# Kernel tuning notes

Hardware: AMD Instinct MI355X
Metric: run time of the kernel (lower is better)

Reference implementation:

```python
import jax, jax.numpy as jnp
import numpy as np

SIZE = (160, 192, 160)  # matches init_kwargs `size`


def _make_grid(size):
    # torch: meshgrid(arange(s) for s, indexing='ij'), stack last dim, flip last dim
    vecs = [jnp.arange(s, dtype=jnp.float32) for s in size]
    g = jnp.stack(jnp.meshgrid(*vecs, indexing='ij'), axis=-1)
    g = g[..., ::-1]  # last-dim order becomes (x, y, z) = (W, H, D) indices
    return g[None]    # [1, D, H, W, 3]


def _grid_sample_3d(src, locs):
    """Trilinear grid_sample, align_corners=True, padding_mode='zeros'.
    src: [B, C, D, H, W]; locs: [B, D, H, W, 3] in [-1,1], last dim (x,y,z)."""
    B, C, D, H, W = src.shape
    dims_m1 = jnp.array([W - 1, H - 1, D - 1], jnp.float32)
    px = (locs + 1.0) * 0.5 * dims_m1  # unnormalize (align_corners=True)
    x, y, z = px[..., 0], px[..., 1], px[..., 2]
    x0 = jnp.floor(x); y0 = jnp.floor(y); z0 = jnp.floor(z)
    fx, fy, fz = x - x0, y - y0, z - z0
    x0i = x0.astype(jnp.int32); y0i = y0.astype(jnp.int32); z0i = z0.astype(jnp.int32)

    def gather(src_b, iz, iy, ix):  # src_b: [C,D,H,W]; idx: [D,H,W]
        return src_b[:, iz, iy, ix]  # [C,D,H,W]

    out = jnp.zeros(src.shape, src.dtype)
    for dz in (0, 1):
        for dy in (0, 1):
            for dx in (0, 1):
                ix, iy, iz = x0i + dx, y0i + dy, z0i + dz
                valid = (ix >= 0) & (ix < W) & (iy >= 0) & (iy < H) & (iz >= 0) & (iz < D)
                w = ((fx if dx else 1.0 - fx)
                     * (fy if dy else 1.0 - fy)
                     * (fz if dz else 1.0 - fz))
                w = jnp.where(valid, w, 0.0)  # zero padding for OOB
                icx = jnp.clip(ix, 0, W - 1)
                icy = jnp.clip(iy, 0, H - 1)
                icz = jnp.clip(iz, 0, D - 1)
                v = jax.vmap(gather)(src, icz, icy, icx)  # [B,C,D,H,W]
                out = out + w[:, None] * v
    return out


def setup_inputs() -> dict:
    key = jax.random.key(0)
    k1, k2 = jax.random.split(key)
    B, C = 2, 2
    D, H, W = SIZE
    src = jax.random.normal(k1, (B, C, D, H, W), dtype=jnp.float32)
    flow = jax.random.normal(k2, (B, 3, D, H, W), dtype=jnp.float32)
    return {"src": src, "flow": flow}


def reference(src, flow):
    # order='image': no flip of flow channels
    flow = jnp.moveaxis(flow, 1, -1)                      # [B,D,H,W,3]
    grid = _make_grid(SIZE)                                # [1,D,H,W,3]
    s = jnp.array(SIZE, jnp.float32)[::-1] - 1.0           # [W-1,H-1,D-1]
    new_locs = 2.0 * ((grid + flow) / s - 0.5)             # normalized [-1,1]
    return _grid_sample_3d(src, new_locs)
```

## Files before the change

kernel.cpp:

```cpp
#include <hip/hip_runtime.h>

#define DD 160
#define HH 192
#define WW 160
#define SP (DD * HH * WW)
#define NB 2
#define NC 2

#define TX 32
#define TY 8
#define TZ 4
#define RXW 40
#define RYH 15
#define RZD 11
#define REGC (RZD * RYH * RXW)
#define NCHUNK (2 * REGC / 4)
#define NITER 13

#define NTX 5
#define NTY 24
#define NTZ 40
#define NTILES (NTX * NTY * NTZ * NB)
#define PER_XCD (NTILES / 8)

typedef float v2f __attribute__((ext_vector_type(2)));
typedef float v4f __attribute__((ext_vector_type(4)));

__device__ __forceinline__ v4f ld4_nt(const float* p) {
    return __builtin_nontemporal_load(reinterpret_cast<const v4f*>(p));
}
__device__ __forceinline__ void st4_nt(float* p, v4f v) {
    __builtin_nontemporal_store(v, reinterpret_cast<v4f*>(p));
}
__device__ __forceinline__ v2f ld2g(const float* p) {
    return *reinterpret_cast<const v2f*>(p);
}

__device__ __forceinline__ void sample_global(
    const float* __restrict__ s0, const float* __restrict__ s1,
    int x, int y, int z, float dx, float dy, float dz,
    float& a0, float& a1)
{
    float sx = (float)x + dx, sy = (float)y + dy, sz = (float)z + dz;
    float xf = floorf(sx), yf = floorf(sy), zf = floorf(sz);
    float fx = sx - xf, fy = sy - yf, fz = sz - zf;
    int x0 = (int)xf, y0 = (int)yf, z0 = (int)zf;
    int x1 = x0 + 1, y1 = y0 + 1, z1 = z0 + 1;

    float wx0 = (x0 >= 0 && x0 < WW) ? (1.0f - fx) : 0.0f;
    float wx1 = (x1 >= 0 && x1 < WW) ? fx : 0.0f;
    float wy0 = (y0 >= 0 && y0 < HH) ? (1.0f - fy) : 0.0f;
    float wy1 = (y1 >= 0 && y1 < HH) ? fy : 0.0f;
    float wz0 = (z0 >= 0 && z0 < DD) ? (1.0f - fz) : 0.0f;
    float wz1 = (z1 >= 0 && z1 < DD) ? fz : 0.0f;

    int p  = min(max(x0, 0), WW - 2);
    int i0 = min(max(x0, 0), WW - 1) - p;
    int i1 = min(max(x1, 0), WW - 1) - p;
    int cy0 = min(max(y0, 0), HH - 1), cy1 = min(max(y1, 0), HH - 1);
    int cz0 = min(max(z0, 0), DD - 1), cz1 = min(max(z1, 0), DD - 1);

    int o00 = (cz0 * HH + cy0) * WW + p;
    int o01 = (cz0 * HH + cy1) * WW + p;
    int o10 = (cz1 * HH + cy0) * WW + p;
    int o11 = (cz1 * HH + cy1) * WW + p;

    float w00 = wz0 * wy0, w01 = wz0 * wy1, w10 = wz1 * wy0, w11 = wz1 * wy1;

    v2f c0_00 = ld2g(s0 + o00); v2f c1_00 = ld2g(s1 + o00);
    v2f c0_01 = ld2g(s0 + o01); v2f c1_01 = ld2g(s1 + o01);
    v2f c0_10 = ld2g(s0 + o10); v2f c1_10 = ld2g(s1 + o10);
    v2f c0_11 = ld2g(s0 + o11); v2f c1_11 = ld2g(s1 + o11);

    #define PICK(v, i) ((i) ? (v).y : (v).x)
    float r0, r1;
    r0  = w00 * (wx0 * PICK(c0_00, i0) + wx1 * PICK(c0_00, i1));
    r1  = w00 * (wx0 * PICK(c1_00, i0) + wx1 * PICK(c1_00, i1));
    r0 += w01 * (wx0 * PICK(c0_01, i0) + wx1 * PICK(c0_01, i1));
    r1 += w01 * (wx0 * PICK(c1_01, i0) + wx1 * PICK(c1_01, i1));
    r0 += w10 * (wx0 * PICK(c0_10, i0) + wx1 * PICK(c0_10, i1));
    r1 += w10 * (wx0 * PICK(c1_10, i0) + wx1 * PICK(c1_10, i1));
    r0 += w11 * (wx0 * PICK(c0_11, i0) + wx1 * PICK(c0_11, i1));
    r1 += w11 * (wx0 * PICK(c1_11, i0) + wx1 * PICK(c1_11, i1));
    #undef PICK
    a0 = r0; a1 = r1;
}

__global__ __launch_bounds__(256, 3) void st_warp_kernel(
    const float* __restrict__ src,
    const float* __restrict__ flow,
    float* __restrict__ out)
{
    __shared__ float sbuf[2 * REGC];

    int u   = blockIdx.x;
    int tl  = (u & 7) * PER_XCD + (u >> 3);
    int tx  = tl % NTX;  int t2 = tl / NTX;
    int ty  = t2 % NTY;  int t3 = t2 / NTY;
    int tz  = t3 % NTZ;  int b  = t3 / NTZ;
    int X0 = tx * TX, Y0 = ty * TY, Z0 = tz * TZ;
    int tid = threadIdx.x;

    const float* sb = src + b * NC * SP;
    const float* s1g = sb + SP;

    v4f vals[NITER];
    int  laddr[NITER];
    #pragma unroll
    for (int i = 0; i < NITER; ++i) {
        int c = tid + i * 256;
        if (i < NITER - 1 || c < NCHUNK) {
            int ch  = (c >= REGC / 4) ? 1 : 0;
            int rem = c - ch * (REGC / 4);
            int lz  = rem / (RYH * RXW / 4);
            int r2  = rem - lz * (RYH * RXW / 4);
            int ly  = r2 / (RXW / 4);
            int lxc = r2 - ly * (RXW / 4);
            int mz = min(max(Z0 - 3 + lz, 0), DD - 1);
            int my = min(max(Y0 - 3 + ly, 0), HH - 1);
            int mx = X0 - 4 + lxc * 4;
            const float* p = sb + ch * SP + (mz * HH + my) * WW;
            v4f v;
            if (mx >= 0 && mx <= WW - 4) {
                v = *reinterpret_cast<const v4f*>(p + mx);
            } else {
                v.x = p[min(max(mx,     0), WW - 1)];
                v.y = p[min(max(mx + 1, 0), WW - 1)];
                v.z = p[min(max(mx + 2, 0), WW - 1)];
                v.w = p[min(max(mx + 3, 0), WW - 1)];
            }
            vals[i]  = v;
            laddr[i] = ch * REGC + (lz * RYH + ly) * RXW + lxc * 4;
        } else {
            laddr[i] = -1;
        }
    }

    int rr = tid >> 3;
    int xi = (tid & 7) << 2;
    int y = Y0 + (rr & 7);
    int z = Z0 + (rr >> 3);
    int x = X0 + xi;
    int fo = b * 3 * SP + (z * HH + y) * WW + x;
    v4f dxv = ld4_nt(flow + fo);
    v4f dyv = ld4_nt(flow + fo + SP);
    v4f dzv = ld4_nt(flow + fo + 2 * SP);

    #pragma unroll
    for (int i = 0; i < NITER; ++i)
        if (laddr[i] >= 0)
            *reinterpret_cast<v4f*>(&sbuf[laddr[i]]) = vals[i];
    __syncthreads();

    const float* c0 = sbuf;
    const float* c1 = sbuf + REGC;
    int rx0 = X0 - 4, ry0 = Y0 - 3, rz0 = Z0 - 3;

    float a0[4], a1[4];
    #pragma unroll
    for (int j = 0; j < 4; ++j) {
        float dx = dxv[j], dy = dyv[j], dz = dzv[j];
        bool inH = (dx >= -4.0f) & (dx < 4.0f) &
                   (dy >= -3.0f) & (dy < 4.0f) &
                   (dz >= -3.0f) & (dz < 4.0f);
        if (inH) {
            float sx = (float)(x + j) + dx;
            float sy = (float)y + dy;
            float sz = (float)z + dz;
            float xf = floorf(sx), yf = floorf(sy), zf = floorf(sz);
            float fx = sx - xf, fy = sy - yf, fz = sz - zf;
            int x0 = (int)xf, y0 = (int)yf, z0 = (int)zf;
            int x1 = x0 + 1, y1 = y0 + 1, z1 = z0 + 1;

            float wx0 = (x0 >= 0 && x0 < WW) ? (1.0f - fx) : 0.0f;
            float wx1 = (x1 >= 0 && x1 < WW) ? fx : 0.0f;
            float wy0 = (y0 >= 0 && y0 < HH) ? (1.0f - fy) : 0.0f;
            float wy1 = (y1 >= 0 && y1 < HH) ? fy : 0.0f;
            float wz0 = (z0 >= 0 && z0 < DD) ? (1.0f - fz) : 0.0f;
            float wz1 = (z1 >= 0 && z1 < DD) ? fz : 0.0f;

            int cx0 = min(max(x0, 0), WW - 1), cx1 = min(max(x1, 0), WW - 1);
            int cy0 = min(max(y0, 0), HH - 1), cy1 = min(max(y1, 0), HH - 1);
            int cz0 = min(max(z0, 0), DD - 1), cz1 = min(max(z1, 0), DD - 1);

            int pb = cx0 - rx0;
            int i1 = cx1 - cx0;
            int ly0 = cy0 - ry0, ly1 = cy1 - ry0;
            int lz0 = cz0 - rz0, lz1 = cz1 - rz0;

            int o00 = (lz0 * RYH + ly0) * RXW + pb;
            int o01 = (lz0 * RYH + ly1) * RXW + pb;
            int o10 = (lz1 * RYH + ly0) * RXW + pb;
            int o11 = (lz1 * RYH + ly1) * RXW + pb;

            float w00 = wz0 * wy0, w01 = wz0 * wy1;
            float w10 = wz1 * wy0, w11 = wz1 * wy1;

            float p00a = c0[o00], p00b = c0[o00 + 1];
            float q00a = c1[o00], q00b = c1[o00 + 1];
            float p01a = c0[o01], p01b = c0[o01 + 1];
            float q01a = c1[o01], q01b = c1[o01 + 1];
            float p10a = c0[o10], p10b = c0[o10 + 1];
            float q10a = c1[o10], q10b = c1[o10 + 1];
            float p11a = c0[o11], p11b = c0[o11 + 1];
            float q11a = c1[o11], q11b = c1[o11 + 1];

            #define SEL(a_, b_) ((i1) ? (b_) : (a_))
            float r0, r1;
            r0  = w00 * (wx0 * p00a + wx1 * SEL(p00a, p00b));
            r1  = w00 * (wx0 * q00a + wx1 * SEL(q00a, q00b));
            r0 += w01 * (wx0 * p01a + wx1 * SEL(p01a, p01b));
            r1 += w01 * (wx0 * q01a + wx1 * SEL(q01a, q01b));
            r0 += w10 * (wx0 * p10a + wx1 * SEL(p10a, p10b));
            r1 += w10 * (wx0 * q10a + wx1 * SEL(q10a, q10b));
            r0 += w11 * (wx0 * p11a + wx1 * SEL(p11a, p11b));
            r1 += w11 * (wx0 * q11a + wx1 * SEL(q11a, q11b));
            #undef SEL
            a0[j] = r0; a1[j] = r1;
        } else {
            sample_global(sb, s1g, x + j, y, z, dx, dy, dz, a0[j], a1[j]);
        }
    }

    int oo = b * NC * SP + (z * HH + y) * WW + x;
    v4f o0 = {a0[0], a0[1], a0[2], a0[3]};
    v4f o1 = {a1[0], a1[1], a1[2], a1[3]};
    st4_nt(out + oo, o0);
    st4_nt(out + oo + SP, o1);
}

extern "C" void kernel_launch(void* const* d_in, const int* in_sizes, int n_in,
                              void* d_out, int out_size, void* d_ws, size_t ws_size,
                              hipStream_t stream) {
    const float* src  = (const float*)d_in[0];
    const float* flow = (const float*)d_in[1];
    float* out = (float*)d_out;

    st_warp_kernel<<<NTILES, 256, 0, stream>>>(src, flow, out);
}
```

Before: 279.8 us.

## Interleave both channels in shared memory and vectorize trilinear interpolation

Shared-memory staging now stores the two source channels interleaved per voxel, so each corner is read with one 8-byte LDS load covering both channels instead of separate scalar reads from two planes. The staging loop loads both channels per chunk, which halves the iteration count while keeping the same register footprint. The interpolation uses local-coordinate indexing without clamping and packed two-wide math, relying on clamped halo values being multiplied by zeroed weights at borders. This cuts LDS instruction count and address arithmetic. In exchange the wider stores may cause bank conflicts, and the boundary handling now depends on the zero-weight logic being correct.

```diff
diff --git a/kernel.cpp b/kernel.cpp
--- a/kernel.cpp
+++ b/kernel.cpp
@@ -14,8 +14,8 @@
 #define RYH 15
 #define RZD 11
 #define REGC (RZD * RYH * RXW)
-#define NCHUNK (2 * REGC / 4)
-#define NITER 13
+#define NCHUNK (REGC / 4)
+#define NITER 7
 
 #define NTX 5
 #define NTY 24
@@ -35,6 +35,7 @@
 __device__ __forceinline__ v2f ld2g(const float* p) {
     return *reinterpret_cast<const v2f*>(p);
 }
+__device__ __forceinline__ v2f s2(float f) { v2f v = {f, f}; return v; }
 
 __device__ __forceinline__ void sample_global(
     const float* __restrict__ s0, const float* __restrict__ s1,
@@ -102,60 +103,59 @@
     int tid = threadIdx.x;
 
     const float* sb = src + b * NC * SP;
-    const float* s1g = sb + SP;
-
-    v4f vals[NITER];
-    int  laddr[NITER];
+
+    v4f va[NITER], vb[NITER];
+    int  ad[NITER];
     #pragma unroll
     for (int i = 0; i < NITER; ++i) {
         int c = tid + i * 256;
         if (i < NITER - 1 || c < NCHUNK) {
-            int ch  = (c >= REGC / 4) ? 1 : 0;
-            int rem = c - ch * (REGC / 4);
-            int lz  = rem / (RYH * RXW / 4);
-            int r2  = rem - lz * (RYH * RXW / 4);
-            int ly  = r2 / (RXW / 4);
-            int lxc = r2 - ly * (RXW / 4);
+            int lz  = c / 150;  int r2 = c - lz * 150;
+            int ly  = r2 / 10;  int lxc = r2 - ly * 10;
             int mz = min(max(Z0 - 3 + lz, 0), DD - 1);
             int my = min(max(Y0 - 3 + ly, 0), HH - 1);
             int mx = X0 - 4 + lxc * 4;
-            const float* p = sb + ch * SP + (mz * HH + my) * WW;
-            v4f v;
+            const float* p = sb + (mz * HH + my) * WW;
+            v4f A, B;
             if (mx >= 0 && mx <= WW - 4) {
-                v = *reinterpret_cast<const v4f*>(p + mx);
+                A = *reinterpret_cast<const v4f*>(p + mx);
+                B = *reinterpret_cast<const v4f*>(p + SP + mx);
             } else {
-                v.x = p[min(max(mx,     0), WW - 1)];
-                v.y = p[min(max(mx + 1, 0), WW - 1)];
-                v.z = p[min(max(mx + 2, 0), WW - 1)];
-                v.w = p[min(max(mx + 3, 0), WW - 1)];
+                int m0 = min(max(mx,     0), WW - 1);
+                int m1 = min(max(mx + 1, 0), WW - 1);
+                int m2 = min(max(mx + 2, 0), WW - 1);
+                int m3 = min(max(mx + 3, 0), WW - 1);
+                A.x = p[m0]; A.y = p[m1]; A.z = p[m2]; A.w = p[m3];
+                B.x = p[SP + m0]; B.y = p[SP + m1]; B.z = p[SP + m2]; B.w = p[SP + m3];
             }
-            vals[i]  = v;
-            laddr[i] = ch * REGC + (lz * RYH + ly) * RXW + lxc * 4;
+            va[i] = A; vb[i] = B;
+            ad[i] = 2 * ((lz * RYH + ly) * RXW + lxc * 4);
         } else {
-            laddr[i] = -1;
+            ad[i] = -1;
         }
     }
 
     int rr = tid >> 3;
     int xi = (tid & 7) << 2;
-    int y = Y0 + (rr & 7);
-    int z = Z0 + (rr >> 3);
-    int x = X0 + xi;
+    int yl = rr & 7, zl = rr >> 3;
+    int y = Y0 + yl, z = Z0 + zl, x = X0 + xi;
     int fo = b * 3 * SP + (z * HH + y) * WW + x;
     v4f dxv = ld4_nt(flow + fo);
     v4f dyv = ld4_nt(flow + fo + SP);
     v4f dzv = ld4_nt(flow + fo + 2 * SP);
 
     #pragma unroll
-    for (int i = 0; i < NITER; ++i)
-        if (laddr[i] >= 0)
-            *reinterpret_cast<v4f*>(&sbuf[laddr[i]]) = vals[i];
+    for (int i = 0; i < NITER; ++i) {
+        if (ad[i] >= 0) {
+            v4f w0 = {va[i].x, vb[i].x, va[i].y, vb[i].y};
+            v4f w1 = {va[i].z, vb[i].z, va[i].w, vb[i].w};
+            *reinterpret_cast<v4f*>(&sbuf[ad[i]])     = w0;
+            *reinterpret_cast<v4f*>(&sbuf[ad[i] + 4]) = w1;
+        }
+    }
     __syncthreads();
 
-    const float* c0 = sbuf;
-    const float* c1 = sbuf + REGC;
-    int rx0 = X0 - 4, ry0 = Y0 - 3, rz0 = Z0 - 3;
-
+    const int rx0 = X0 - 4, ry0 = Y0 - 3, rz0 = Z0 - 3;
     float a0[4], a1[4];
     #pragma unroll
     for (int j = 0; j < 4; ++j) {
@@ -164,61 +164,42 @@
                    (dy >= -3.0f) & (dy < 4.0f) &
                    (dz >= -3.0f) & (dz < 4.0f);
         if (inH) {
-            float sx = (float)(x + j) + dx;
-            float sy = (float)y + dy;
-            float sz = (float)z + dz;
-            float xf = floorf(sx), yf = floorf(sy), zf = floorf(sz);
-            float fx = sx - xf, fy = sy - yf, fz = sz - zf;
-            int x0 = (int)xf, y0 = (int)yf, z0 = (int)zf;
-            int x1 = x0 + 1, y1 = y0 + 1, z1 = z0 + 1;
-
-            float wx0 = (x0 >= 0 && x0 < WW) ? (1.0f - fx) : 0.0f;
-            float wx1 = (x1 >= 0 && x1 < WW) ? fx : 0.0f;
-            float wy0 = (y0 >= 0 && y0 < HH) ? (1.0f - fy) : 0.0f;
-            float wy1 = (y1 >= 0 && y1 < HH) ? fy : 0.0f;
-            float wz0 = (z0 >= 0 && z0 < DD) ? (1.0f - fz) : 0.0f;
-            float wz1 = (z1 >= 0 && z1 < DD) ? fz : 0.0f;
-
-            int cx0 = min(max(x0, 0), WW - 1), cx1 = min(max(x1, 0), WW - 1);
-            int cy0 = min(max(y0, 0), HH - 1), cy1 = min(max(y1, 0), HH - 1);
-            int cz0 = min(max(z0, 0), DD - 1), cz1 = min(max(z1, 0), DD - 1);
-
-            int pb = cx0 - rx0;
-            int i1 = cx1 - cx0;
-            int ly0 = cy0 - ry0, ly1 = cy1 - ry0;
-            int lz0 = cz0 - rz0, lz1 = cz1 - rz0;
-
-            int o00 = (lz0 * RYH + ly0) * RXW + pb;
-            int o01 = (lz0 * RYH + ly1) * RXW + pb;
-            int o10 = (lz1 * RYH + ly0) * RXW + pb;
-            int o11 = (lz1 * RYH + ly1) * RXW + pb;
-
-            float w00 = wz0 * wy0, w01 = wz0 * wy1;
-            float w10 = wz1 * wy0, w11 = wz1 * wy1;
-
-            float p00a = c0[o00], p00b = c0[o00 + 1];
-            float q00a = c1[o00], q00b = c1[o00 + 1];
-            float p01a = c0[o01], p01b = c0[o01 + 1];
-            float q01a = c1[o01], q01b = c1[o01 + 1];
-            float p10a = c0[o10], p10b = c0[o10 + 1];
-            float q10a = c1[o10], q10b = c1[o10 + 1];
-            float p11a = c0[o11], p11b = c0[o11 + 1];
-            float q11a = c1[o11], q11b = c1[o11 + 1];
-
-            #define SEL(a_, b_) ((i1) ? (b_) : (a_))
-            float r0, r1;
-            r0  = w00 * (wx0 * p00a + wx1 * SEL(p00a, p00b));
-            r1  = w00 * (wx0 * q00a + wx1 * SEL(q00a, q00b));
-            r0 += w01 * (wx0 * p01a + wx1 * SEL(p01a, p01b));
-            r1 += w01 * (wx0 * q01a + wx1 * SEL(q01a, q01b));
-            r0 += w10 * (wx0 * p10a + wx1 * SEL(p10a, p10b));
-            r1 += w10 * (wx0 * q10a + wx1 * SEL(q10a, q10b));
-            r0 += w11 * (wx0 * p11a + wx1 * SEL(p11a, p11b));
-            r1 += w11 * (wx0 * q11a + wx1 * SEL(q11a, q11b));
-            #undef SEL
-            a0[j] = r0; a1[j] = r1;
+            float lx = (float)(xi + j + 4) + dx;
+            float ly = (float)(yl + 3) + dy;
+            float lz = (float)(zl + 3) + dz;
+            float xf = floorf(lx), yf = floorf(ly), zf = floorf(lz);
+            float fx = lx - xf, fy = ly - yf, fz = lz - zf;
+            int ix = (int)xf, iy = (int)yf, iz = (int)zf;
+
+            int vx0 = ix + rx0, vy0 = iy + ry0, vz0 = iz + rz0;
+            float wx0 = (vx0 >= 0  && vx0 < WW)     ? (1.0f - fx) : 0.0f;
+            float wx1 = (vx0 >= -1 && vx0 < WW - 1) ? fx          : 0.0f;
+            float wy0 = (vy0 >= 0  && vy0 < HH)     ? (1.0f - fy) : 0.0f;
+            float wy1 = (vy0 >= -1 && vy0 < HH - 1) ? fy          : 0.0f;
+            float wz0 = (vz0 >= 0  && vz0 < DD)     ? (1.0f - fz) : 0.0f;
+            float wz1 = (vz0 >= -1 && vz0 < DD - 1) ? fz          : 0.0f;
+
+            const float* pB = sbuf + 2 * ((iz * RYH + iy) * RXW + ix);
+            v2f A00 = *(const v2f*)(pB);
+            v2f B00 = *(const v2f*)(pB + 2);
+            v2f A01 = *(const v2f*)(pB + 2 * RXW);
+            v2f B01 = *(const v2f*)(pB + 2 * RXW + 2);
+            const float* pC = pB + 2 * RYH * RXW;
+            v2f A10 = *(const v2f*)(pC);
+            v2f B10 = *(const v2f*)(pC + 2);
+            v2f A11 = *(const v2f*)(pC + 2 * RXW);
+            v2f B11 = *(const v2f*)(pC + 2 * RXW + 2);
+
+            v2f c00 = s2(wx0) * A00 + s2(wx1) * B00;
+            v2f c01 = s2(wx0) * A01 + s2(wx1) * B01;
+            v2f c10 = s2(wx0) * A10 + s2(wx1) * B10;
+            v2f c11 = s2(wx0) * A11 + s2(wx1) * B11;
+            v2f m0  = s2(wy0) * c00 + s2(wy1) * c01;
+            v2f m1  = s2(wy0) * c10 + s2(wy1) * c11;
+            v2f r   = s2(wz0) * m0  + s2(wz1) * m1;
+            a0[j] = r.x; a1[j] = r.y;
         } else {
-            sample_global(sb, s1g, x + j, y, z, dx, dy, dz, a0[j], a1[j]);
+            sample_global(sb, sb + SP, x + j, y, z, dx, dy, dz, a0[j], a1[j]);
         }
     }
 
```

Result: faster. 273.6 us (-2.2%).
